# Kernel tuning notes

Measured on AMD Instinct MI355X. Metric: run time of the kernel, lower is better.

## Reference

```python
import jax, jax.numpy as jnp
import numpy as np

N_NODES = 50000
N_EDGES = 800000
D = 128
N_LAYERS = 5
N_REL = 500
N_ENT = 50000  # fc output size (num_entities)
BATCH = 1024


def setup_inputs() -> dict:
    key = jax.random.key(0)
    ks = jax.random.split(key, 10)
    return {
        "entity_embed": jax.random.normal(ks[0], (N_NODES, D), dtype=jnp.float32),
        "edge_val": jnp.ones((N_EDGES,), dtype=jnp.float32),
        "gnn_W": jax.random.normal(ks[1], (N_LAYERS, D, D), dtype=jnp.float32) * (1.0 / np.sqrt(D)),
        "gnn_b": jax.random.normal(ks[2], (N_LAYERS, D), dtype=jnp.float32) * 0.01,
        "rel_table": jax.random.normal(ks[3], (N_REL, D), dtype=jnp.float32),
        "fc_W": jax.random.normal(ks[4], (2 * D, N_ENT), dtype=jnp.float32) * (1.0 / np.sqrt(2 * D)),
        "fc_b": jax.random.normal(ks[5], (N_ENT,), dtype=jnp.float32) * 0.01,
        "edge_row": jax.random.randint(ks[6], (N_EDGES,), 0, N_NODES, dtype=jnp.int32),
        "edge_col": jax.random.randint(ks[7], (N_EDGES,), 0, N_NODES, dtype=jnp.int32),
        "head_idx": jax.random.randint(ks[8], (BATCH,), 0, N_NODES, dtype=jnp.int32),
        "rel_ids": jax.random.randint(ks[9], (BATCH,), 0, N_REL, dtype=jnp.int32),
    }


def reference(entity_embed, edge_val, gnn_W, gnn_b, rel_table, fc_W, fc_b,
              edge_row, edge_col, head_idx, rel_ids):
    n_nodes = entity_embed.shape[0]

    def layer(x, wb):
        W, b = wb
        # sparse.mm(adj, x): out[row] += val * x[col]
        msgs = edge_val[:, None] * x[edge_col]          # [E, D]
        agg = jax.ops.segment_sum(msgs, edge_row, num_segments=n_nodes)  # [N, D]
        return jax.nn.relu(agg @ W + b), None

    all_embed, _ = jax.lax.scan(layer, entity_embed, (gnn_W, gnn_b))

    head_embed = all_embed[head_idx]                    # [B, D]
    rel_embed = rel_table[rel_ids]                      # [B, D]
    embed = jnp.concatenate([head_embed, rel_embed], axis=1)  # [B, 2D]
    logits = embed @ fc_W + fc_b                        # [B, N_ENT]
    return logits
```

## Files before the change

kernel.cpp:

```cpp
#include <hip/hip_runtime.h>


#define N_NODES 50000
#define N_EDGES 800000
#define D 128
#define N_LAYERS 5
#define N_ENT 50000
#define BATCH 1024
#define KDIM 256
#define SCAN_BLOCKS ((N_NODES + 255) / 256)
#define FC_NT 64

typedef __attribute__((ext_vector_type(8))) __bf16 bf16x8;
typedef __attribute__((ext_vector_type(4))) float f32x4;
typedef __attribute__((ext_vector_type(8))) unsigned short u16x8;
typedef __attribute__((ext_vector_type(4))) unsigned short u16x4;

__device__ inline unsigned short f2bf(float x) {
  unsigned int u = __float_as_uint(x);
  unsigned int r = (u + 0x7FFFu + ((u >> 16) & 1u)) >> 16;
  return (unsigned short)r;
}
__device__ inline float bf2f(unsigned short b) {
  return __uint_as_float(((unsigned int)b) << 16);
}

__global__ void zero_i32(int* __restrict__ p, int n) {
  int i = blockIdx.x * blockDim.x + threadIdx.x;
  if (i < n) p[i] = 0;
}

__global__ void hist_kernel(const int* __restrict__ rows, int* __restrict__ counts) {
  int i = blockIdx.x * blockDim.x + threadIdx.x;
  int stride = gridDim.x * blockDim.x;
  for (; i < N_EDGES; i += stride) atomicAdd(&counts[rows[i]], 1);
}

__device__ inline int block_exscan256(int v, int* wsum, int* tot) {
  int t = threadIdx.x, lane = t & 63, wid = t >> 6;
  int s = v;
#pragma unroll
  for (int off = 1; off < 64; off <<= 1) {
    int u = __shfl_up(s, off, 64);
    if (lane >= off) s += u;
  }
  if (lane == 63) wsum[wid] = s;
  __syncthreads();
  if (t == 0) {
    int run = 0;
#pragma unroll
    for (int w = 0; w < 4; ++w) { int tmp = wsum[w]; wsum[w] = run; run += tmp; }
    wsum[4] = run;
  }
  __syncthreads();
  *tot = wsum[4];
  return wsum[wid] + s - v;
}

__global__ __launch_bounds__(256) void scan1_kernel(const int* __restrict__ counts,
                                                    int* __restrict__ row_ptr,
                                                    int* __restrict__ bsum) {
  __shared__ int wsum[5];
  int i = blockIdx.x * 256 + threadIdx.x;
  int v = (i < N_NODES) ? counts[i] : 0;
  int tot;
  int ex = block_exscan256(v, wsum, &tot);
  if (i < N_NODES) row_ptr[i] = ex;
  if (threadIdx.x == 0) bsum[blockIdx.x] = tot;
}

__global__ __launch_bounds__(256) void scan2_kernel(int* __restrict__ bsum) {
  __shared__ int wsum[5];
  int t = threadIdx.x;
  int v = (t < SCAN_BLOCKS) ? bsum[t] : 0;
  int tot;
  int ex = block_exscan256(v, wsum, &tot);
  if (t < SCAN_BLOCKS) bsum[t] = ex;
}

__global__ __launch_bounds__(256) void scan3_kernel(const int* __restrict__ counts,
                                                    const int* __restrict__ bsum,
                                                    int* __restrict__ row_ptr,
                                                    int* __restrict__ cursor) {
  int i = blockIdx.x * 256 + threadIdx.x;
  if (i >= N_NODES) return;
  int ex = row_ptr[i] + bsum[blockIdx.x];
  row_ptr[i] = ex;
  cursor[i] = ex;
  if (i == N_NODES - 1) row_ptr[N_NODES] = ex + counts[i];
}

__global__ void scatter_kernel(const int* __restrict__ rows, const int* __restrict__ cols,
                               const float* __restrict__ vals, int* __restrict__ cursor,
                               int* __restrict__ col_s, float* __restrict__ val_s) {
  int i = blockIdx.x * blockDim.x + threadIdx.x;
  int stride = gridDim.x * blockDim.x;
  for (; i < N_EDGES; i += stride) {
    int r = rows[i];
    int pos = atomicAdd(&cursor[r], 1);
    col_s[pos] = cols[i];
    val_s[pos] = vals[i];
  }
}

__global__ __launch_bounds__(256) void tobf16_kernel(const float* __restrict__ src,
                                                     unsigned short* __restrict__ dst,
                                                     int n8) {
  int i = blockIdx.x * blockDim.x + threadIdx.x;
  if (i >= n8) return;
  float4 a = *(const float4*)&src[i * 8];
  float4 b = *(const float4*)&src[i * 8 + 4];
  u16x8 o;
  o[0] = f2bf(a.x); o[1] = f2bf(a.y); o[2] = f2bf(a.z); o[3] = f2bf(a.w);
  o[4] = f2bf(b.x); o[5] = f2bf(b.y); o[6] = f2bf(b.z); o[7] = f2bf(b.w);
  *(u16x8*)&dst[i * 8] = o;
}

__global__ void wconv_kernel(const float* __restrict__ gW, unsigned short* __restrict__ Wt5) {
  int idx = blockIdx.x * 256 + threadIdx.x;
  if (idx >= N_LAYERS * D * D) return;
  int l = idx / (D * D);
  int rem = idx - l * D * D;
  int j = rem >> 7;
  int k = rem & 127;
  Wt5[idx] = f2bf(gW[l * D * D + k * D + j]);
}

__device__ inline void agg_batch(int cl, float vl, int cnt, int q, int l16,
                                 const unsigned short* __restrict__ xb, float* acc) {
  int j = 0;
  for (; j + 4 <= cnt; j += 4) {
    int c[4]; float v[4]; u16x8 xv[4];
#pragma unroll
    for (int u = 0; u < 4; ++u) {
      c[u] = __shfl(cl, q * 16 + j + u);
      v[u] = __shfl(vl, q * 16 + j + u);
    }
#pragma unroll
    for (int u = 0; u < 4; ++u) xv[u] = *(const u16x8*)&xb[c[u] * D + l16 * 8];
#pragma unroll
    for (int u = 0; u < 4; ++u)
#pragma unroll
      for (int dd = 0; dd < 8; ++dd) acc[dd] = fmaf(v[u], bf2f(xv[u][dd]), acc[dd]);
  }
  for (; j < cnt; ++j) {
    int c = __shfl(cl, q * 16 + j);
    float v = __shfl(vl, q * 16 + j);
    u16x8 xv0 = *(const u16x8*)&xb[c * D + l16 * 8];
#pragma unroll
    for (int dd = 0; dd < 8; ++dd) acc[dd] = fmaf(v, bf2f(xv0[dd]), acc[dd]);
  }
}

__global__ __launch_bounds__(256) void layer_fused(const unsigned short* __restrict__ xb,
                                                   const int* __restrict__ row_ptr,
                                                   const int* __restrict__ cols,
                                                   const float* __restrict__ vals,
                                                   const unsigned short* __restrict__ Bt,
                                                   const float* __restrict__ bias,
                                                   unsigned short* __restrict__ yb) {
  __shared__ unsigned short atile[64 * D];
  int t = threadIdx.x, lane = t & 63, wave = t >> 6;
  int q = lane >> 4, l16 = lane & 15;
  int r0 = blockIdx.x * 64;
  char* ab = (char*)atile;

#pragma unroll
  for (int p = 0; p < 4; ++p) {
    int row_l = wave * 16 + p * 4 + q;
    int r = r0 + row_l;
    float acc[8] = {0.f, 0.f, 0.f, 0.f, 0.f, 0.f, 0.f, 0.f};
    if (r < N_NODES) {
      int e0 = row_ptr[r], e1 = row_ptr[r + 1];
      for (int base = e0; base < e1; base += 16) {
        int idx = base + l16;
        bool ok = idx < e1;
        int cl = ok ? cols[idx] : 0;
        float vl = ok ? vals[idx] : 0.f;
        agg_batch(cl, vl, min(16, e1 - base), q, l16, xb, acc);
      }
    }
    u16x8 o;
#pragma unroll
    for (int dd = 0; dd < 8; ++dd) o[dd] = f2bf(acc[dd]);
    *(u16x8*)(ab + row_l * 256 + ((l16 ^ (row_l & 7)) << 4)) = o;
  }
  __syncthreads();

  int lq = lane >> 4;
  f32x4 acc2[4][2];
#pragma unroll
  for (int m = 0; m < 4; ++m) { acc2[m][0] = (f32x4){0,0,0,0}; acc2[m][1] = (f32x4){0,0,0,0}; }
#pragma unroll
  for (int kk = 0; kk < 4; ++kk) {
    bf16x8 wfr[2];
#pragma unroll
    for (int nt = 0; nt < 2; ++nt)
      wfr[nt] = *(const bf16x8*)&Bt[(wave * 32 + nt * 16 + l16) * D + kk * 32 + lq * 8];
#pragma unroll
    for (int m = 0; m < 4; ++m) {
      int row_l = m * 16 + l16;
      bf16x8 afr = *(const bf16x8*)(ab + row_l * 256 + ((((kk * 4 + lq) ^ (row_l & 7)) << 4)));
      acc2[m][0] = __builtin_amdgcn_mfma_f32_16x16x32_bf16(wfr[0], afr, acc2[m][0], 0, 0, 0);
      acc2[m][1] = __builtin_amdgcn_mfma_f32_16x16x32_bf16(wfr[1], afr, acc2[m][1], 0, 0, 0);
    }
  }
#pragma unroll
  for (int nt = 0; nt < 2; ++nt) {
    int jb = wave * 32 + nt * 16 + lq * 4;
    float4 bb = *(const float4*)&bias[jb];
#pragma unroll
    for (int m = 0; m < 4; ++m) {
      int r = r0 + m * 16 + l16;
      if (r < N_NODES) {
        u16x4 o;
        o[0] = f2bf(fmaxf(acc2[m][nt][0] + bb.x, 0.f));
        o[1] = f2bf(fmaxf(acc2[m][nt][1] + bb.y, 0.f));
        o[2] = f2bf(fmaxf(acc2[m][nt][2] + bb.z, 0.f));
        o[3] = f2bf(fmaxf(acc2[m][nt][3] + bb.w, 0.f));
        *(u16x4*)&yb[(size_t)r * D + jb] = o;
      }
    }
  }
}

__global__ __launch_bounds__(256) void layer_head(const unsigned short* __restrict__ xb,
                                                  const int* __restrict__ row_ptr,
                                                  const int* __restrict__ cols,
                                                  const float* __restrict__ vals,
                                                  const int* __restrict__ head_idx,
                                                  const float* __restrict__ rel_table,
                                                  const int* __restrict__ rel_ids,
                                                  const unsigned short* __restrict__ Bt,
                                                  const float* __restrict__ bias,
                                                  unsigned short* __restrict__ ebf) {
  __shared__ unsigned short atile[64 * D];
  int t = threadIdx.x, lane = t & 63, wave = t >> 6;
  int q = lane >> 4, l16 = lane & 15;
  int r0 = blockIdx.x * 64;
  char* ab = (char*)atile;

#pragma unroll
  for (int it = 0; it < 4; ++it) {
    int c = it * 256 + t;
    int bl = c >> 4;
    int kq = c & 15;
    int b = r0 + bl;
    const float* rp = &rel_table[(size_t)rel_ids[b] * D + kq * 8];
    float4 a0 = *(const float4*)rp;
    float4 a1 = *(const float4*)(rp + 4);
    u16x8 o;
    o[0] = f2bf(a0.x); o[1] = f2bf(a0.y); o[2] = f2bf(a0.z); o[3] = f2bf(a0.w);
    o[4] = f2bf(a1.x); o[5] = f2bf(a1.y); o[6] = f2bf(a1.z); o[7] = f2bf(a1.w);
    *(u16x8*)&ebf[(size_t)b * KDIM + D + kq * 8] = o;
  }

#pragma unroll
  for (int p = 0; p < 4; ++p) {
    int row_l = wave * 16 + p * 4 + q;
    int b = r0 + row_l;
    int r = head_idx[b];
    float acc[8] = {0.f, 0.f, 0.f, 0.f, 0.f, 0.f, 0.f, 0.f};
    int e0 = row_ptr[r], e1 = row_ptr[r + 1];
    for (int base = e0; base < e1; base += 16) {
      int idx = base + l16;
      bool ok = idx < e1;
      int cl = ok ? cols[idx] : 0;
      float vl = ok ? vals[idx] : 0.f;
      agg_batch(cl, vl, min(16, e1 - base), q, l16, xb, acc);
    }
    u16x8 o;
#pragma unroll
    for (int dd = 0; dd < 8; ++dd) o[dd] = f2bf(acc[dd]);
    *(u16x8*)(ab + row_l * 256 + ((l16 ^ (row_l & 7)) << 4)) = o;
  }
  __syncthreads();

  int lq = lane >> 4;
  f32x4 acc2[4][2];
#pragma unroll
  for (int m = 0; m < 4; ++m) { acc2[m][0] = (f32x4){0,0,0,0}; acc2[m][1] = (f32x4){0,0,0,0}; }
#pragma unroll
  for (int kk = 0; kk < 4; ++kk) {
    bf16x8 wfr[2];
#pragma unroll
    for (int nt = 0; nt < 2; ++nt)
      wfr[nt] = *(const bf16x8*)&Bt[(wave * 32 + nt * 16 + l16) * D + kk * 32 + lq * 8];
#pragma unroll
    for (int m = 0; m < 4; ++m) {
      int row_l = m * 16 + l16;
      bf16x8 afr = *(const bf16x8*)(ab + row_l * 256 + ((((kk * 4 + lq) ^ (row_l & 7)) << 4)));
      acc2[m][0] = __builtin_amdgcn_mfma_f32_16x16x32_bf16(wfr[0], afr, acc2[m][0], 0, 0, 0);
      acc2[m][1] = __builtin_amdgcn_mfma_f32_16x16x32_bf16(wfr[1], afr, acc2[m][1], 0, 0, 0);
    }
  }
#pragma unroll
  for (int nt = 0; nt < 2; ++nt) {
    int jb = wave * 32 + nt * 16 + lq * 4;
    float4 bb = *(const float4*)&bias[jb];
#pragma unroll
    for (int m = 0; m < 4; ++m) {
      int b = r0 + m * 16 + l16;
      u16x4 o;
      o[0] = f2bf(fmaxf(acc2[m][nt][0] + bb.x, 0.f));
      o[1] = f2bf(fmaxf(acc2[m][nt][1] + bb.y, 0.f));
      o[2] = f2bf(fmaxf(acc2[m][nt][2] + bb.z, 0.f));
      o[3] = f2bf(fmaxf(acc2[m][nt][3] + bb.w, 0.f));
      *(u16x4*)&ebf[(size_t)b * KDIM + jb] = o;
    }
  }
}

__global__ __launch_bounds__(256) void wt_kernel(const float* __restrict__ fcW,
                                                 unsigned short* __restrict__ Wt) {
  int n = blockIdx.x * 256 + threadIdx.x;
  int k0 = blockIdx.y * 8;
  if (n >= N_ENT) return;
  u16x8 pk;
#pragma unroll
  for (int e = 0; e < 8; ++e) pk[e] = f2bf(fcW[(size_t)(k0 + e) * N_ENT + n]);
  *(u16x8*)&Wt[(size_t)n * KDIM + k0] = pk;
}

__global__ __launch_bounds__(256, 4) void fc_mfma(const unsigned short* __restrict__ ebf,
                                                  const unsigned short* __restrict__ Wt,
                                                  const float* __restrict__ fcb,
                                                  float* __restrict__ out) {
  __shared__ unsigned short etile[64 * KDIM];
  int t = threadIdx.x;
  int lane = t & 63, wave = t >> 6;
  int l16 = lane & 15, lq = lane >> 4;
  int n0 = blockIdx.x * FC_NT;
  char* eb = (char*)etile;

  bf16x8 afr[8];
  {
    const unsigned short* wp = Wt + (size_t)(n0 + wave * 16 + l16) * KDIM + lq * 8;
#pragma unroll
    for (int kk = 0; kk < 8; ++kk) afr[kk] = *(const bf16x8*)(wp + kk * 32);
  }

  int n_st = n0 + wave * 16 + lq * 4;
  bool nok = n_st < N_ENT;
  float4 bv = make_float4(0.f, 0.f, 0.f, 0.f);
  if (nok) bv = *(const float4*)&fcb[n_st];

  for (int bc = 0; bc < 8; ++bc) {
    int b0 = blockIdx.y * 512 + bc * 64;
    const char* esrc = (const char*)(ebf + (size_t)b0 * KDIM);
#pragma unroll
    for (int it = 0; it < 8; ++it) {
      int c = it * 256 + t;
      int row = c >> 5;
      int ci = c & 31;
      float4 v = *(const float4*)(esrc + (size_t)c * 16);
      *(float4*)(eb + row * 512 + ((ci ^ ((row & 7) << 2)) << 4)) = v;
    }
    __syncthreads();

    f32x4 acc[4];
#pragma unroll
    for (int m = 0; m < 4; ++m) acc[m] = (f32x4){0.f, 0.f, 0.f, 0.f};

#pragma unroll
    for (int m = 0; m < 4; ++m) {
      int row = m * 16 + l16;
#pragma unroll
      for (int kk = 0; kk < 8; ++kk) {
        bf16x8 bfr = *(const bf16x8*)(eb + row * 512 + ((((kk * 4 + lq) ^ ((row & 7) << 2)) << 4)));
        acc[m] = __builtin_amdgcn_mfma_f32_16x16x32_bf16(afr[kk], bfr, acc[m], 0, 0, 0);
      }
    }

    if (nok) {
#pragma unroll
      for (int m = 0; m < 4; ++m) {
        int b = b0 + m * 16 + l16;
        float4 o = {acc[m][0] + bv.x, acc[m][1] + bv.y, acc[m][2] + bv.z, acc[m][3] + bv.w};
        *(float4*)&out[(size_t)b * N_ENT + n_st] = o;
      }
    }
    __syncthreads();
  }
}

extern "C" void kernel_launch(void* const* d_in, const int* in_sizes, int n_in,
                              void* d_out, int out_size, void* d_ws, size_t ws_size,
                              hipStream_t stream) {
  const float* entity    = (const float*)d_in[0];
  const float* edge_val  = (const float*)d_in[1];
  const float* gnn_W     = (const float*)d_in[2];
  const float* gnn_b     = (const float*)d_in[3];
  const float* rel_table = (const float*)d_in[4];
  const float* fc_W      = (const float*)d_in[5];
  const float* fc_b      = (const float*)d_in[6];
  const int* edge_row    = (const int*)d_in[7];
  const int* edge_col    = (const int*)d_in[8];
  const int* head_idx    = (const int*)d_in[9];
  const int* rel_ids     = (const int*)d_in[10];
  float* out = (float*)d_out;

  char* ws = (char*)d_ws;
  size_t off = 0;
  auto alloc = [&](size_t bytes) -> void* {
    void* p = ws + off;
    off = (off + bytes + 255) & ~(size_t)255;
    return p;
  };
  int* counts   = (int*)alloc((size_t)N_NODES * 4);
  int* row_ptr  = (int*)alloc((size_t)(N_NODES + 1) * 4);
  int* cursor   = (int*)alloc((size_t)N_NODES * 4);
  int* bsum     = (int*)alloc((size_t)256 * 4);
  int* col_s    = (int*)alloc((size_t)N_EDGES * 4);
  float* val_s  = (float*)alloc((size_t)N_EDGES * 4);
  unsigned short* xA    = (unsigned short*)alloc((size_t)N_NODES * D * 2);
  unsigned short* xB    = (unsigned short*)alloc((size_t)N_NODES * D * 2);
  unsigned short* entbf = (unsigned short*)alloc((size_t)N_NODES * D * 2);
  unsigned short* ebf   = (unsigned short*)alloc((size_t)BATCH * KDIM * 2);
  unsigned short* Wt    = (unsigned short*)alloc((size_t)(N_ENT + 256) * KDIM * 2);
  unsigned short* Wt5   = (unsigned short*)alloc((size_t)N_LAYERS * D * D * 2);

  zero_i32<<<(N_NODES + 255) / 256, 256, 0, stream>>>(counts, N_NODES);
  hist_kernel<<<1024, 256, 0, stream>>>(edge_row, counts);
  scan1_kernel<<<SCAN_BLOCKS, 256, 0, stream>>>(counts, row_ptr, bsum);
  scan2_kernel<<<1, 256, 0, stream>>>(bsum);
  scan3_kernel<<<SCAN_BLOCKS, 256, 0, stream>>>(counts, bsum, row_ptr, cursor);
  scatter_kernel<<<1024, 256, 0, stream>>>(edge_row, edge_col, edge_val, cursor, col_s, val_s);

  tobf16_kernel<<<(N_NODES * D / 8 + 255) / 256, 256, 0, stream>>>(entity, entbf, N_NODES * D / 8);
  wconv_kernel<<<(N_LAYERS * D * D + 255) / 256, 256, 0, stream>>>(gnn_W, Wt5);

  for (int layer = 0; layer < N_LAYERS - 1; ++layer) {
    const unsigned short* xin = (layer == 0) ? entbf : ((layer & 1) ? xA : xB);
    unsigned short* yout = (layer & 1) ? xB : xA;
    layer_fused<<<(N_NODES + 63) / 64, 256, 0, stream>>>(xin, row_ptr, col_s, val_s,
                                                         Wt5 + (size_t)layer * D * D,
                                                         gnn_b + (size_t)layer * D, yout);
  }

  dim3 wtg((N_ENT + 255) / 256, KDIM / 8);
  wt_kernel<<<wtg, 256, 0, stream>>>(fc_W, Wt);

  layer_head<<<BATCH / 64, 256, 0, stream>>>(xB, row_ptr, col_s, val_s, head_idx,
                                             rel_table, rel_ids,
                                             Wt5 + (size_t)(N_LAYERS - 1) * D * D,
                                             gnn_b + (size_t)(N_LAYERS - 1) * D, ebf);

  dim3 fcg((N_ENT + FC_NT - 1) / FC_NT, 2);
  fc_mfma<<<fcg, 256, 0, stream>>>(ebf, Wt, fc_b, out);
}
```

Before: 385.4 us.

## Double-buffer embedding tiles in fc_mfma with register prefetch

The FC MFMA kernel now keeps two LDS buffers for the embedding tile and preloads the next 64-row chunk into registers while the current chunk is being computed. The register data is written to the alternate buffer after compute, so each iteration needs one barrier instead of two. The change doubles LDS use to 64KB per block, uses more registers, and lowers the occupancy hint in launch bounds from 4 to 2 blocks per CU.

```diff
diff --git a/kernel.cpp b/kernel.cpp
--- a/kernel.cpp
+++ b/kernel.cpp
@@ -322,16 +322,15 @@
   *(u16x8*)&Wt[(size_t)n * KDIM + k0] = pk;
 }
 
-__global__ __launch_bounds__(256, 4) void fc_mfma(const unsigned short* __restrict__ ebf,
+__global__ __launch_bounds__(256, 2) void fc_mfma(const unsigned short* __restrict__ ebf,
                                                   const unsigned short* __restrict__ Wt,
                                                   const float* __restrict__ fcb,
                                                   float* __restrict__ out) {
-  __shared__ unsigned short etile[64 * KDIM];
+  __shared__ unsigned short etile[2][64 * KDIM];
   int t = threadIdx.x;
   int lane = t & 63, wave = t >> 6;
   int l16 = lane & 15, lq = lane >> 4;
   int n0 = blockIdx.x * FC_NT;
-  char* eb = (char*)etile;
 
   bf16x8 afr[8];
   {
@@ -345,18 +344,39 @@
   float4 bv = make_float4(0.f, 0.f, 0.f, 0.f);
   if (nok) bv = *(const float4*)&fcb[n_st];
 
+  int srow[8], soff[8];
+#pragma unroll
+  for (int it = 0; it < 8; ++it) {
+    int c = it * 256 + t;
+    int row = c >> 5;
+    int ci = c & 31;
+    srow[it] = row;
+    soff[it] = row * 512 + ((ci ^ ((row & 7) << 2)) << 4);
+  }
+
+  {
+    const char* esrc = (const char*)(ebf + (size_t)(blockIdx.y * 512) * KDIM);
+    char* eb0 = (char*)etile[0];
+#pragma unroll
+    for (int it = 0; it < 8; ++it) {
+      float4 v = *(const float4*)(esrc + (size_t)(it * 256 + t) * 16);
+      *(float4*)(eb0 + soff[it]) = v;
+    }
+  }
+  __syncthreads();
+
   for (int bc = 0; bc < 8; ++bc) {
+    char* eb = (char*)etile[bc & 1];
     int b0 = blockIdx.y * 512 + bc * 64;
-    const char* esrc = (const char*)(ebf + (size_t)b0 * KDIM);
-#pragma unroll
-    for (int it = 0; it < 8; ++it) {
-      int c = it * 256 + t;
-      int row = c >> 5;
-      int ci = c & 31;
-      float4 v = *(const float4*)(esrc + (size_t)c * 16);
-      *(float4*)(eb + row * 512 + ((ci ^ ((row & 7) << 2)) << 4)) = v;
-    }
-    __syncthreads();
+
+    float4 nxt[8];
+    bool have_next = (bc + 1) < 8;
+    if (have_next) {
+      const char* esrc = (const char*)(ebf + (size_t)(b0 + 64) * KDIM);
+#pragma unroll
+      for (int it = 0; it < 8; ++it)
+        nxt[it] = *(const float4*)(esrc + (size_t)(it * 256 + t) * 16);
+    }
 
     f32x4 acc[4];
 #pragma unroll
@@ -379,6 +399,13 @@
         float4 o = {acc[m][0] + bv.x, acc[m][1] + bv.y, acc[m][2] + bv.z, acc[m][3] + bv.w};
         *(float4*)&out[(size_t)b * N_ENT + n_st] = o;
       }
+    }
+
+    if (have_next) {
+      char* ebn = (char*)etile[(bc + 1) & 1];
+#pragma unroll
+      for (int it = 0; it < 8; ++it)
+        *(float4*)(ebn + soff[it]) = nxt[it];
     }
     __syncthreads();
   }
```

Measured after the change: 391.9 us. Within noise of the previous version (+1.7%).
